# Performance work log

Measured on AMD Instinct MI355X. Metric: run time of the kernel, lower is better.

## Reference

```python
import jax, jax.numpy as jnp
import numpy as np

B, C_IN, H, W_SP = 16, 128, 56, 56
C_OUT, KH, KW = 256, 3, 3
STRIDE = (1, 1)
PADDING = (1, 1)


def setup_inputs() -> dict:
    key = jax.random.key(0)
    kx, kw = jax.random.split(key)
    x = jax.random.normal(kx, (B, C_IN, H, W_SP), dtype=jnp.float32)
    W = jax.random.normal(kw, (C_OUT, C_IN, KH, KW), dtype=jnp.float32) * 0.01
    b = jnp.zeros((C_OUT,), dtype=jnp.float32)
    return {"x": x, "W": W, "b": b}


def reference(x, W, b):
    # NCHW direct convolution, same math as the nested-loop torch module.
    out = jax.lax.conv_general_dilated(
        x, W,
        window_strides=STRIDE,
        padding=[(PADDING[0], PADDING[0]), (PADDING[1], PADDING[1])],
        dimension_numbers=("NCHW", "OIHW", "NCHW"),
    )
    return out + b[None, :, None, None]
```

## Files before the change

### kernel.cpp

```cpp
#include <hip/hip_runtime.h>

typedef __attribute__((ext_vector_type(8))) short short8;
typedef __attribute__((ext_vector_type(4))) float f32x4;

#define CI    128
#define CO_   256
#define HW_   56
#define PLANE 3136
#define NB    16
#define STOT  50176
#define KTOT  1152
#define OUTN  802816
#define PLSZ  3211264ull

#define XT_BYTES   12845056ull
#define WP_USHORTS 294912
#define WS_NEED    (12845056ull + 589824ull + 256ull)

__device__ __forceinline__ unsigned short f2bf(float f) {
  unsigned u = __float_as_uint(f);
  u += 0x7FFFu + ((u >> 16) & 1u);
  return (unsigned short)(u >> 16);
}

__device__ __forceinline__ void gload16(void* lds, const void* g) {
  __builtin_amdgcn_global_load_lds(
      (const __attribute__((address_space(1))) unsigned int*)g,
      (__attribute__((address_space(3))) unsigned int*)lds, 16, 0, 0);
}

template <int N> __device__ __forceinline__ void vmwait() {
  asm volatile("s_waitcnt vmcnt(%0)" ::"n"(N) : "memory");
}

__global__ __launch_bounds__(256) void prep_fused(const float* __restrict__ X,
                                                  const float* __restrict__ W,
                                                  unsigned short* __restrict__ Xt,
                                                  unsigned short* __restrict__ Wp) {
  const int t = threadIdx.x;
  if (blockIdx.x < 1600) {
    __shared__ __align__(16) unsigned short tile[32][132];
    const int bx = blockIdx.x;
    const int n   = bx / 100;
    const int rem = bx % 100;
    const int cib = rem / 25;
    const int spb = rem % 25;
    const int sp0 = spb * 128;
    const float* src = X + (size_t)(n * CI + cib * 32) * PLANE;
#pragma unroll
    for (int j = 0; j < 4; ++j) {
      int f = t + 256 * j;
      int ci  = f >> 5;
      int sp4 = (f & 31) * 4;
      if (sp0 + sp4 < PLANE) {
        f32x4 v = *(const f32x4*)(src + (size_t)ci * PLANE + sp0 + sp4);
#pragma unroll
        for (int e = 0; e < 4; ++e) tile[ci][sp4 + e] = f2bf(v[e]);
      }
    }
    __syncthreads();
    unsigned short* dstp = Xt + (size_t)cib * (PLSZ / 2) + ((size_t)n * PLANE + sp0) * 32;
#pragma unroll
    for (int j = 0; j < 2; ++j) {
      int g = t + 256 * j;
      int sp = g >> 2;
      int q  = g & 3;
      if (sp0 + sp < PLANE) {
        short8 v;
#pragma unroll
        for (int e = 0; e < 8; ++e) v[e] = (short)tile[q * 8 + e][sp];
        *(short8*)(dstp + (size_t)sp * 32 + q * 8) = v;
      }
    }
  } else {
    const int u = (blockIdx.x - 1600) * 256 + t;
    const int rcbmt = u >> 9;
    const int p     = u & 511;
    const int mt  = rcbmt & 1;
    const int rcb = rcbmt >> 1;
    const int cb  = rcb & 3;
    const int r   = rcb >> 2;
    const int col = p >> 2;
    const int kg  = (p & 3) ^ ((col >> 1) & 3);
    const int co  = mt * 128 + col;
    const int ci0 = cb * 32 + kg * 8;
    short8 v;
#pragma unroll
    for (int e = 0; e < 8; ++e)
      v[e] = (short)f2bf(W[(size_t)co * KTOT + (size_t)(ci0 + e) * 9 + r]);
    *(short8*)(Wp + (size_t)u * 8) = v;
    if (u < 16) {
      short8 z = {0, 0, 0, 0, 0, 0, 0, 0};
      *(short8*)(Wp + WP_USHORTS + u * 8) = z;
    }
  }
}

__global__ __launch_bounds__(256, 3) void conv_gemm(const unsigned short* __restrict__ Xt,
                                                    const unsigned short* __restrict__ Wp,
                                                    const float* __restrict__ bias,
                                                    float* __restrict__ out) {
  __shared__ __align__(1024) char smem[49152];
  const int t    = threadIdx.x;
  const int lane = t & 63;
  const int wid  = t >> 6;
  const int wm   = wid >> 1, wn = wid & 1;

  int bx = blockIdx.x;
  bx = (bx & 7) * 98 + (bx >> 3);
  const int mt  = bx & 1;
  const int spt = bx >> 1;

  const int kgB = (lane & 3) ^ ((lane >> 3) & 3);
  const int S0 = spt * 128 + wid * 32 + (lane >> 2);
  const int S1 = S0 + 16;
  const int hw0 = S0 % PLANE, h0 = hw0 / HW_, w0 = hw0 - h0 * HW_;
  const int hw1 = S1 % PLANE, h1 = hw1 / HW_, w1 = hw1 - h1 * HW_;
  int vm0 = 0, vm1 = 0;
#pragma unroll
  for (int r = 0; r < 9; ++r) {
    int dh = r / 3 - 1, dw = r % 3 - 1;
    vm0 |= (int)(((unsigned)(h0 + dh) < HW_) & ((unsigned)(w0 + dw) < HW_)) << r;
    vm1 |= (int)(((unsigned)(h1 + dh) < HW_) & ((unsigned)(w1 + dw) < HW_)) << r;
  }
  const char* xb0 = (const char*)Xt + (size_t)S0 * 64 + kgB * 16;
  const char* xb1 = (const char*)Xt + (size_t)S1 * 64 + kgB * 16;
  const char* zb  = (const char*)(Wp + WP_USHORTS) + (lane & 3) * 16;
  const char* wpA = (const char*)Wp + mt * 8192 + t * 16;

  const int swz  = ((lane >> 4) ^ ((lane >> 1) & 3)) * 16;
  const int aoff = (wm * 64 + (lane & 15)) * 64 + swz;
  const int boff = 8192 + (wn * 64 + (lane & 15)) * 64 + swz;

  f32x4 acc[4][4];
  const f32x4 zf = {0.f, 0.f, 0.f, 0.f};
#pragma unroll
  for (int m = 0; m < 4; ++m)
#pragma unroll
    for (int n = 0; n < 4; ++n) acc[m][n] = zf;

  auto STAGE = [&](int s1) {
    char* buf = smem + (s1 % 3) * 16384;
    const int r = s1 >> 2, cb = s1 & 3;
    const int dh = r / 3 - 1, dw = r % 3 - 1;
    const long  ro = (long)(dh * HW_ + dw) * 64 + (long)cb * PLSZ;
    const char* as = wpA + r * 65536 + cb * 16384;
    char* abuf = buf + wid * 1024;
    gload16(abuf, as);
    gload16(abuf + 4096, as + 4096);
    const bool v0 = (vm0 >> r) & 1;
    const bool v1 = (vm1 >> r) & 1;
    gload16(buf + 8192 + wid * 2048,        v0 ? xb0 + ro : zb);
    gload16(buf + 8192 + wid * 2048 + 1024, v1 ? xb1 + ro : zb);
  };

  STAGE(0); STAGE(1); STAGE(2);

#pragma unroll
  for (int s = 0; s < 36; ++s) {
    if (s <= 33)      vmwait<8>();
    else if (s == 34) vmwait<4>();
    else              vmwait<0>();
    __builtin_amdgcn_s_barrier();

    const char* rb = smem + (s % 3) * 16384;
    short8 a[4], b[4];
#pragma unroll
    for (int m = 0; m < 4; ++m) a[m] = *(const short8*)(rb + aoff + m * 1024);
#pragma unroll
    for (int n = 0; n < 4; ++n) b[n] = *(const short8*)(rb + boff + n * 1024);

    __builtin_amdgcn_s_setprio(1);
#pragma unroll
    for (int m = 0; m < 4; ++m)
#pragma unroll
      for (int n = 0; n < 4; ++n)
        acc[m][n] = __builtin_amdgcn_mfma_f32_16x16x32_bf16(a[m], b[n], acc[m][n], 0, 0, 0);
    __builtin_amdgcn_s_setprio(0);

    if (s < 33) {
      __builtin_amdgcn_s_barrier();
      STAGE(s + 3);
    }
  }

#pragma unroll
  for (int nf = 0; nf < 4; ++nf) {
    int S = spt * 128 + wn * 64 + nf * 16 + (lane & 15);
    int nimg = S / PLANE, hw = S - nimg * PLANE;
    float* ob = out + (size_t)nimg * OUTN + hw;
#pragma unroll
    for (int mf = 0; mf < 4; ++mf) {
      int cob = mt * 128 + wm * 64 + mf * 16 + (lane >> 4) * 4;
#pragma unroll
      for (int r2 = 0; r2 < 4; ++r2)
        ob[(size_t)(cob + r2) * PLANE] = acc[mf][nf][r2] + bias[cob + r2];
    }
  }
}

__global__ __launch_bounds__(256) void conv_naive(const float* __restrict__ X,
                                                  const float* __restrict__ W,
                                                  const float* __restrict__ bias,
                                                  float* __restrict__ out) {
  int idx = blockIdx.x * 256 + threadIdx.x;
  int hw = idx % PLANE;
  int co = (idx / PLANE) & 255;
  int n  = idx / (PLANE * 256);
  int h = hw / HW_, w = hw - h * HW_;
  float acc = bias[co];
  const float* xp = X + (size_t)n * CI * PLANE;
  const float* wp = W + (size_t)co * KTOT;
  for (int ci = 0; ci < CI; ++ci) {
#pragma unroll
    for (int kh = 0; kh < 3; ++kh) {
      int y = h + kh - 1;
      if ((unsigned)y >= HW_) continue;
#pragma unroll
      for (int kw = 0; kw < 3; ++kw) {
        int x = w + kw - 1;
        if ((unsigned)x >= HW_) continue;
        acc += xp[(size_t)ci * PLANE + y * HW_ + x] * wp[ci * 9 + kh * 3 + kw];
      }
    }
  }
  out[idx] = acc;
}

extern "C" void kernel_launch(void* const* d_in, const int* in_sizes, int n_in,
                              void* d_out, int out_size, void* d_ws, size_t ws_size,
                              hipStream_t stream) {
  (void)in_sizes; (void)n_in; (void)out_size;
  const float* X = (const float*)d_in[0];
  const float* W = (const float*)d_in[1];
  const float* b = (const float*)d_in[2];
  float* out = (float*)d_out;
  if (ws_size >= WS_NEED) {
    unsigned short* Xt = (unsigned short*)d_ws;
    unsigned short* Wp = (unsigned short*)((char*)d_ws + XT_BYTES);
    prep_fused<<<1744, 256, 0, stream>>>(X, W, Xt, Wp);
    conv_gemm<<<784, 256, 0, stream>>>(Xt, Wp, b, out);
  } else {
    conv_naive<<<(NB * CO_ * PLANE + 255) / 256, 256, 0, stream>>>(X, W, b, out);
  }
}
```

Measured before the change: 50.32 us.

## Load weight fragments directly into registers, bypassing LDS staging

The weight prep kernel now writes weights in MFMA fragment order per wave and lane. The GEMM kernel then loads its A operand straight from global memory into a three-deep register ring, prefetched two stages ahead. Only the input tile is staged through LDS, which halves shared memory and removes the A-side LDS reads. In exchange it uses about 48 more VGPRs and repeats weight loads from global or L2 for both waves that share a row, and the vmcnt accounting has to match the new load counts.

After: 58.02 us. +15.3%, slower.

```diff
diff --git a/kernel.cpp b/kernel.cpp
--- a/kernel.cpp
+++ b/kernel.cpp
@@ -74,16 +74,16 @@
     }
   } else {
     const int u = (blockIdx.x - 1600) * 256 + t;
-    const int rcbmt = u >> 9;
-    const int p     = u & 511;
-    const int mt  = rcbmt & 1;
-    const int rcb = rcbmt >> 1;
-    const int cb  = rcb & 3;
-    const int r   = rcb >> 2;
-    const int col = p >> 2;
-    const int kg  = (p & 3) ^ ((col >> 1) & 3);
-    const int co  = mt * 128 + col;
-    const int ci0 = cb * 32 + kg * 8;
+    const int sub = u >> 9;
+    const int c   = u & 511;
+    const int mt  = sub & 1;
+    const int cb  = (sub >> 1) & 3;
+    const int r   = sub >> 3;
+    const int wmh = c >> 8;
+    const int m   = (c >> 6) & 3;
+    const int ln  = c & 63;
+    const int co  = mt * 128 + wmh * 64 + m * 16 + (ln & 15);
+    const int ci0 = cb * 32 + (ln >> 4) * 8;
     short8 v;
 #pragma unroll
     for (int e = 0; e < 8; ++e)
@@ -100,7 +100,7 @@
                                                     const unsigned short* __restrict__ Wp,
                                                     const float* __restrict__ bias,
                                                     float* __restrict__ out) {
-  __shared__ __align__(1024) char smem[49152];
+  __shared__ __align__(1024) char smem[24576];
   const int t    = threadIdx.x;
   const int lane = t & 63;
   const int wid  = t >> 6;
@@ -126,11 +126,10 @@
   const char* xb0 = (const char*)Xt + (size_t)S0 * 64 + kgB * 16;
   const char* xb1 = (const char*)Xt + (size_t)S1 * 64 + kgB * 16;
   const char* zb  = (const char*)(Wp + WP_USHORTS) + (lane & 3) * 16;
-  const char* wpA = (const char*)Wp + mt * 8192 + t * 16;
+  const char* wpAL = (const char*)Wp + mt * 8192 + wm * 4096 + lane * 16;
 
   const int swz  = ((lane >> 4) ^ ((lane >> 1) & 3)) * 16;
-  const int aoff = (wm * 64 + (lane & 15)) * 64 + swz;
-  const int boff = 8192 + (wn * 64 + (lane & 15)) * 64 + swz;
+  const int boff = (wn * 64 + (lane & 15)) * 64 + swz;
 
   f32x4 acc[4][4];
   const f32x4 zf = {0.f, 0.f, 0.f, 0.f};
@@ -139,34 +138,39 @@
 #pragma unroll
     for (int n = 0; n < 4; ++n) acc[m][n] = zf;
 
-  auto STAGE = [&](int s1) {
-    char* buf = smem + (s1 % 3) * 16384;
+  short8 a3[3][4];
+
+  auto STAGE_B = [&](int s1) {
+    char* buf = smem + (s1 % 3) * 8192;
     const int r = s1 >> 2, cb = s1 & 3;
     const int dh = r / 3 - 1, dw = r % 3 - 1;
-    const long  ro = (long)(dh * HW_ + dw) * 64 + (long)cb * PLSZ;
-    const char* as = wpA + r * 65536 + cb * 16384;
-    char* abuf = buf + wid * 1024;
-    gload16(abuf, as);
-    gload16(abuf + 4096, as + 4096);
+    const long ro = (long)(dh * HW_ + dw) * 64 + (long)cb * PLSZ;
     const bool v0 = (vm0 >> r) & 1;
     const bool v1 = (vm1 >> r) & 1;
-    gload16(buf + 8192 + wid * 2048,        v0 ? xb0 + ro : zb);
-    gload16(buf + 8192 + wid * 2048 + 1024, v1 ? xb1 + ro : zb);
+    gload16(buf + wid * 2048,        v0 ? xb0 + ro : zb);
+    gload16(buf + wid * 2048 + 1024, v1 ? xb1 + ro : zb);
   };
-
-  STAGE(0); STAGE(1); STAGE(2);
+#define A_PREF(S1)                                                                \
+  {                                                                               \
+    const char* ab_ = wpAL + (size_t)(S1) * 16384;                                \
+    _Pragma("unroll") for (int m = 0; m < 4; ++m)                                 \
+      a3[(S1) % 3][m] = *(const short8*)(ab_ + m * 1024);                         \
+  }
+
+  STAGE_B(0); STAGE_B(1);
+  A_PREF(0)
+  STAGE_B(2);
+  A_PREF(1)
 
 #pragma unroll
   for (int s = 0; s < 36; ++s) {
-    if (s <= 33)      vmwait<8>();
+    if (s <= 33)      vmwait<6>();
     else if (s == 34) vmwait<4>();
     else              vmwait<0>();
     __builtin_amdgcn_s_barrier();
 
-    const char* rb = smem + (s % 3) * 16384;
-    short8 a[4], b[4];
-#pragma unroll
-    for (int m = 0; m < 4; ++m) a[m] = *(const short8*)(rb + aoff + m * 1024);
+    const char* rb = smem + (s % 3) * 8192;
+    short8 b[4];
 #pragma unroll
     for (int n = 0; n < 4; ++n) b[n] = *(const short8*)(rb + boff + n * 1024);
 
@@ -175,13 +179,14 @@
     for (int m = 0; m < 4; ++m)
 #pragma unroll
       for (int n = 0; n < 4; ++n)
-        acc[m][n] = __builtin_amdgcn_mfma_f32_16x16x32_bf16(a[m], b[n], acc[m][n], 0, 0, 0);
+        acc[m][n] = __builtin_amdgcn_mfma_f32_16x16x32_bf16(a3[s % 3][m], b[n], acc[m][n], 0, 0, 0);
     __builtin_amdgcn_s_setprio(0);
 
     if (s < 33) {
       __builtin_amdgcn_s_barrier();
-      STAGE(s + 3);
-    }
+      STAGE_B(s + 3);
+    }
+    if (s <= 33) A_PREF(s + 2)
   }
 
 #pragma unroll
```
